# Kernel tuning notes

Hardware: AMD Instinct MI355X
Metric: run time of the kernel (lower is better)

Reference implementation:

```python
import jax, jax.numpy as jnp
import numpy as np

C = 64
CQ = C // 4
G = 8  # group norm groups
EPS_GN = 1e-5
POS_COEF = 0.1


def setup_inputs() -> dict:
    key = jax.random.key(0)
    ks = jax.random.split(key, 12)
    B, N = 2, 4096
    return {
        "context_features": jax.random.normal(ks[0], (B, C, N), jnp.float32),
        "motion_features": jax.random.normal(ks[1], (B, C, N), jnp.float32),
        "xyz1": jax.random.uniform(ks[2], (B, N, 3), jnp.float32),
        # tied q/k conv weight (Conv1d k=1, no bias): (C//4, C)
        "Wqk": jax.random.normal(ks[3], (CQ, C), jnp.float32) * 0.1,
        # v_conv: Conv1d(C, C, 1) with bias
        "Wv": jax.random.normal(ks[4], (C, C), jnp.float32) * 0.1,
        "bv": jax.random.normal(ks[5], (C,), jnp.float32) * 0.1,
        # trans_conv: Conv1d(C, C, 1) with bias
        "Wt": jax.random.normal(ks[6], (C, C), jnp.float32) * 0.1,
        "bt": jax.random.normal(ks[7], (C,), jnp.float32) * 0.1,
        # GroupNorm(8, C) affine params
        "gn_w": jax.random.normal(ks[8], (C,), jnp.float32) * 0.1 + 1.0,
        "gn_b": jax.random.normal(ks[9], (C,), jnp.float32) * 0.1,
        # PReLU single slope, alpha_gma scalar (init 0 in torch; random here for testing)
        "prelu_a": jnp.float32(0.25) + jax.random.normal(ks[10], (), jnp.float32) * 0.01,
        "alpha": jax.random.normal(ks[11], (), jnp.float32) * 0.1,
    }


def _group_norm(x, w, b):
    # x: (B, C, N)
    B, Cc, N = x.shape
    xg = x.reshape(B, G, Cc // G, N)
    mu = xg.mean(axis=(2, 3), keepdims=True)
    var = xg.var(axis=(2, 3), keepdims=True)
    xn = ((xg - mu) * jax.lax.rsqrt(var + EPS_GN)).reshape(B, Cc, N)
    return xn * w[None, :, None] + b[None, :, None]


def reference(context_features, motion_features, xyz1, Wqk, Wv, bv, Wt, bt, gn_w, gn_b, prelu_a, alpha):
    # --- self attention (tied q/k) ---
    q = jnp.einsum("oc,bcn->bon", Wqk, context_features)  # (B, C/4, N)
    corr = jnp.einsum("bom,bon->bmn", q, q)               # (B, N, N)
    attn = jax.nn.softmax(corr, axis=-1)
    attn = attn / (1e-9 + attn.sum(axis=1, keepdims=True))

    # --- position mask via Gram-trick squared distances ---
    sq = jnp.sum(xyz1 * xyz1, axis=-1)                    # (B, N)
    d = sq[:, :, None] + sq[:, None, :] - 2.0 * jnp.einsum("bid,bjd->bij", xyz1, xyz1)
    d = jnp.maximum(d, 0.0)
    pos_am = d / (1e-9 + d.sum(axis=1, keepdims=True))
    mask = pos_am <= POS_COEF

    local = attn * mask
    local = jax.nn.softmax(local, axis=-1)
    local = local / (1e-9 + local.sum(axis=1, keepdims=True))
    attn = attn + local

    # --- GMA fusion ---
    xv = jnp.einsum("oc,bcn->bon", Wv, motion_features) + bv[None, :, None]
    gma = jnp.einsum("bcm,bmn->bcn", xv, attn)
    res = jnp.einsum("oc,bcn->bon", Wt, motion_features - gma) + bt[None, :, None]
    gr = _group_norm(res, gn_w, gn_b)
    gr = jnp.where(gr >= 0, gr, prelu_a * gr)  # PReLU
    return alpha * gr + motion_features
```

## Files before the change

### kernel.cpp

```cpp
#include <hip/hip_runtime.h>
#include <hip/hip_bf16.h>
#include <cstdio>

#define NB 2
#define NN 4096
#define NC 64
#define NQ 16
#define POS_COEF 0.1f

#define OFF_QT   0u
#define OFF_QK   131072u
#define OFF_XYZ4 262144u
#define OFF_XYZK 294912u
#define OFF_IRS1 327680u
#define OFF_IRS2 335872u
#define OFF_THR  344064u
#define OFF_ICS1 352256u
#define OFF_FLAG 360448u
#define OFF_XVB  360464u
#define OFF_SUMS 622608u
#define OFF_GN   622616u
#define OFF_CS2  622648u
#define OFF_GMA  630840u
#define OFF_G2   1155128u
// ... 242 lines not shown
    const float* __restrict__ irs1, const float* __restrict__ ics1,
    const float* __restrict__ thr, float* __restrict__ irs2) {
  const int tid = threadIdx.x;
  const int b = blockIdx.x >> 8;
  const int m0 = (blockIdx.x & 255) << 4;
  const int w = tid >> 6, lane = tid & 63;
  const float* qb = qt + (size_t)b * NN * 16;
  const float* kb = qk + (size_t)b * 16 * NN;
  const float* xk = xyzk + (size_t)b * 4 * NN;
  const int mA = m0 + w, mB = m0 + w + 4, mC = m0 + w + 8, mD = m0 + w + 12;
  LQROW(ma, qb + (size_t)mA * 16)
  LQROW(mb, qb + (size_t)mB * 16)
  LQROW(mc, qb + (size_t)mC * 16)
  LQROW(md, qb + (size_t)mD * 16)
  const float4 pmA = *(const float4*)(xyz4 + ((size_t)b * NN + mA) * 4);
  const float4 pmB = *(const float4*)(xyz4 + ((size_t)b * NN + mB) * 4);
  const float4 pmC = *(const float4*)(xyz4 + ((size_t)b * NN + mC) * 4);
  const float4 pmD = *(const float4*)(xyz4 + ((size_t)b * NN + mD) * 4);
  const float rA = irs1[b * NN + mA];
  const float rB = irs1[b * NN + mB];
  const float rC = irs1[b * NN + mC];
  const float rD = irs1[b * NN + mD];
  float sA = 0.f, sB = 0.f, sC = 0.f, sD = 0.f;
#define P3C(S, M0,M1,M2,M3, PM, R, C) { \
    float corr_ = DOTC(M0,M1,M2,M3,C); \
    float a1v_ = __expf(fminf(corr_, 80.f)) * (R) * ic.C; \
    float dd_ = (PM).w + pw.C - 2.f * ((PM).x * px.C + (PM).y * py.C + (PM).z * pz.C); \
    dd_ = fmaxf(dd_, 0.f); \
    float l0_ = (dd_ <= th.C) ? a1v_ : 0.f; \
    S += __expf(l0_); }
  for (int it = 0; it < 16; ++it) {
    const int n0 = (it << 8) + (lane << 2);
    LKPL(kb, n0)
    const float4 px = *(const float4*)(xk + 0*NN + n0);
    const float4 py = *(const float4*)(xk + 1*NN + n0);
    const float4 pz = *(const float4*)(xk + 2*NN + n0);
    const float4 pw = *(const float4*)(xk + 3*NN + n0);
    const float4 ic = *(const float4*)(ics1 + b * NN + n0);
    const float4 th = *(const float4*)(thr + b * NN + n0);
    P3C(sA, ma0,ma1,ma2,ma3, pmA, rA, x)
    P3C(sA, ma0,ma1,ma2,ma3, pmA, rA, y)
    P3C(sA, ma0,ma1,ma2,ma3, pmA, rA, z)
    P3C(sA, ma0,ma1,ma2,ma3, pmA, rA, w)
    P3C(sB, mb0,mb1,mb2,mb3, pmB, rB, x)
    P3C(sB, mb0,mb1,mb2,mb3, pmB, rB, y)
    P3C(sB, mb0,mb1,mb2,mb3, pmB, rB, z)
    P3C(sB, mb0,mb1,mb2,mb3, pmB, rB, w)
    P3C(sC, mc0,mc1,mc2,mc3, pmC, rC, x)
    P3C(sC, mc0,mc1,mc2,mc3, pmC, rC, y)
    P3C(sC, mc0,mc1,mc2,mc3, pmC, rC, z)
    P3C(sC, mc0,mc1,mc2,mc3, pmC, rC, w)
    P3C(sD, md0,md1,md2,md3, pmD, rD, x)
    P3C(sD, md0,md1,md2,md3, pmD, rD, y)
    P3C(sD, md0,md1,md2,md3, pmD, rD, z)
    P3C(sD, md0,md1,md2,md3, pmD, rD, w)
  }
#undef P3C
  WRED(sA) WRED(sB) WRED(sC) WRED(sD)
  if (lane == 0) {
    irs2[b * NN + mA] = rcpf_(sA);
    irs2[b * NN + mB] = rcpf_(sB);
    irs2[b * NN + mC] = rcpf_(sC);
    irs2[b * NN + mD] = rcpf_(sD);
  }
}

__global__ __launch_bounds__(256) void k7_gma(
    const float* __restrict__ qt, const float* __restrict__ xyz4,
    const unsigned short* __restrict__ xvb,
    const float* __restrict__ irs1, const float* __restrict__ irs2,
    const float* __restrict__ ics1, const float* __restrict__ thr,
    float* __restrict__ g1, float* __restrict__ g2, float* __restrict__ cs2) {
  const int tid = threadIdx.x;
  const int bid = blockIdx.x;
  const int msl = bid & 7;
  const int nb = (bid >> 3) & 63;
  const int b = bid >> 9;
  const int n0 = nb << 6;
  const int mstart = msl << 9;
  __shared__ __align__(16) unsigned short attns1[64 * 72];
  __shared__ __align__(16) unsigned short attns2[64 * 72];
  __shared__ __align__(16) unsigned short xvs[64 * 72];
  const float* qb = qt + (size_t)b * NN * 16;
  const float* pb = xyz4 + (size_t)b * NN * 4;
  const int ni = tid & 63, aw = tid >> 6;
  const int na = n0 + ni;
  const float* qnp = qb + (size_t)na * 16;
  LQROW(q, qnp)
  const float4 pn = *(const float4*)(pb + (size_t)na * 4);
  const float ics1n = ics1[b * NN + na];
  const float thr_n = thr[b * NN + na];
  const int lane = tid & 63, wv = tid >> 6;
  const int lr = lane & 15, quad = lane >> 4;
  const int nw = wv << 4;
  f32x4v acc0 = {0,0,0,0}, acc1 = {0,0,0,0}, acc2 = {0,0,0,0}, acc3 = {0,0,0,0};
  f32x4v d0 = {0,0,0,0}, d1 = {0,0,0,0}, d2 = {0,0,0,0}, d3 = {0,0,0,0};
  float csacc = 0.f;
#define COMPA(MOFF, D1, D2) { \
    const int m_ = __builtin_amdgcn_readfirstlane(mw + (MOFF)); \
    const float* qm_ = qb + (size_t)m_ * 16; \
    LQROW(wq, qm_) \
    float corr_ = DOT16M(q0, q1, q2, q3, wq0, wq1, wq2, wq3); \
    const float4 pm_ = *(const float4*)(pb + (size_t)m_ * 4); \
    float a1v_ = __expf(fminf(corr_, 80.f)) * irs1[b * NN + m_] * ics1n; \
    float dd_ = pm_.w + pn.w - 2.f * (pm_.x * pn.x + pm_.y * pn.y + pm_.z * pn.z); \
    dd_ = fmaxf(dd_, 0.f); \
    float l0_ = (dd_ <= thr_n) ? a1v_ : 0.f; \
    float l2n_ = __expf(l0_) * irs2[b * NN + m_]; \
    D1 = f2bf(a1v_); D2 = f2bf(l2n_); csacc += l2n_; }
  for (int mt = 0; mt < 8; ++mt) {
    const int m0 = mstart + (mt << 6);
    __syncthreads();
    {
      const int c = tid >> 2, part = tid & 3;
      const unsigned short* src = xvb + ((size_t)b * 64 + c) * NN + m0 + part * 16;
      unsigned short* dst = xvs + c * 72 + part * 16;
      *(uint4*)dst = *(const uint4*)src;
      *(uint4*)(dst + 8) = *(const uint4*)(src + 8);
    }
    const int mw = m0 + (aw << 4);
#pragma unroll
    for (int g = 0; g < 4; ++g) {
      ushort4 u1, u2;
      COMPA(g * 4 + 0, u1.x, u2.x)
      COMPA(g * 4 + 1, u1.y, u2.y)
      COMPA(g * 4 + 2, u1.z, u2.z)
      COMPA(g * 4 + 3, u1.w, u2.w)
      *(ushort4*)(attns1 + ni * 72 + (aw << 4) + (g << 2)) = u1;
      *(ushort4*)(attns2 + ni * 72 + (aw << 4) + (g << 2)) = u2;
    }
    __syncthreads();
#pragma unroll
    for (int h = 0; h < 2; ++h) {
      const bf16x8 a1 = *(const bf16x8*)(attns1 + (nw + lr) * 72 + h * 32 + quad * 8);
      const bf16x8 a2 = *(const bf16x8*)(attns2 + (nw + lr) * 72 + h * 32 + quad * 8);
      const bf16x8 b0 = *(const bf16x8*)(xvs + (lr) * 72 + h * 32 + quad * 8);
      const bf16x8 b1 = *(const bf16x8*)(xvs + (16 + lr) * 72 + h * 32 + quad * 8);
      const bf16x8 b2 = *(const bf16x8*)(xvs + (32 + lr) * 72 + h * 32 + quad * 8);
      const bf16x8 b3 = *(const bf16x8*)(xvs + (48 + lr) * 72 + h * 32 + quad * 8);
      acc0 = __builtin_amdgcn_mfma_f32_16x16x32_bf16(a1, b0, acc0, 0, 0, 0);
      acc1 = __builtin_amdgcn_mfma_f32_16x16x32_bf16(a1, b1, acc1, 0, 0, 0);
      acc2 = __builtin_amdgcn_mfma_f32_16x16x32_bf16(a1, b2, acc2, 0, 0, 0);
      acc3 = __builtin_amdgcn_mfma_f32_16x16x32_bf16(a1, b3, acc3, 0, 0, 0);
      d0 = __builtin_amdgcn_mfma_f32_16x16x32_bf16(a2, b0, d0, 0, 0, 0);
      d1 = __builtin_amdgcn_mfma_f32_16x16x32_bf16(a2, b1, d1, 0, 0, 0);
      d2 = __builtin_amdgcn_mfma_f32_16x16x32_bf16(a2, b2, d2, 0, 0, 0);
      d3 = __builtin_amdgcn_mfma_f32_16x16x32_bf16(a2, b3, d3, 0, 0, 0);
    }
  }
#undef COMPA
  atomicAdd(&cs2[b * NN + na], csacc);
#define EPI(ACC, DST, CT) { \
    float* g_ = (DST) + ((size_t)b * NN + n0 + nw + (quad << 2)) * 64 + (CT) * 16 + lr; \
    atomicAdd(g_ + 0,   ACC[0]); \
    atomicAdd(g_ + 64,  ACC[1]); \
    atomicAdd(g_ + 128, ACC[2]); \
    atomicAdd(g_ + 192, ACC[3]); }
  EPI(acc0, g1, 0) EPI(acc1, g1, 1) EPI(acc2, g1, 2) EPI(acc3, g1, 3)
  EPI(d0, g2, 0) EPI(d1, g2, 1) EPI(d2, g2, 2) EPI(d3, g2, 3)
#undef EPI
}


__global__ __launch_bounds__(256) void p1w_rs1(
    const float* __restrict__ qt, const float* __restrict__ qk,
    float* __restrict__ irs1, unsigned short* __restrict__ a0g) {
  const int tid = threadIdx.x;
  const int b = blockIdx.x >> 8;
  const int m0 = (blockIdx.x & 255) << 4;
  const int w = tid >> 6, lane = tid & 63;
  const float* qb = qt + (size_t)b * NN * 16;
  const float* kb = qk + (size_t)b * 16 * NN;
  unsigned short* ab = a0g + (size_t)b * NN * NN;
  const int mA = m0 + w, mB = m0 + w + 4, mC = m0 + w + 8, mD = m0 + w + 12;
  LQROW(ma, qb + (size_t)mA * 16)
  LQROW(mb, qb + (size_t)mB * 16)
  LQROW(mc, qb + (size_t)mC * 16)
  LQROW(md, qb + (size_t)mD * 16)
  float sA = 0.f, sB = 0.f, sC = 0.f, sD = 0.f;
#define P1E(S, U, UC, M0,M1,M2,M3, C) { \
    float e_ = __expf(fminf(DOTC(M0,M1,M2,M3,C), 80.f)); \
    unsigned short us_ = f2bf(e_); U.UC = us_; S += bf2f(us_); }
  for (int it = 0; it < 16; ++it) {
    const int n0 = (it << 8) + (lane << 2);
    LKPL(kb, n0)
    ushort4 uA, uB, uC, uD;
    P1E(sA, uA, x, ma0,ma1,ma2,ma3, x) P1E(sA, uA, y, ma0,ma1,ma2,ma3, y)
    P1E(sA, uA, z, ma0,ma1,ma2,ma3, z) P1E(sA, uA, w, ma0,ma1,ma2,ma3, w)
    P1E(sB, uB, x, mb0,mb1,mb2,mb3, x) P1E(sB, uB, y, mb0,mb1,mb2,mb3, y)
    P1E(sB, uB, z, mb0,mb1,mb2,mb3, z) P1E(sB, uB, w, mb0,mb1,mb2,mb3, w)
    P1E(sC, uC, x, mc0,mc1,mc2,mc3, x) P1E(sC, uC, y, mc0,mc1,mc2,mc3, y)
    P1E(sC, uC, z, mc0,mc1,mc2,mc3, z) P1E(sC, uC, w, mc0,mc1,mc2,mc3, w)
    P1E(sD, uD, x, md0,md1,md2,md3, x) P1E(sD, uD, y, md0,md1,md2,md3, y)
    P1E(sD, uD, z, md0,md1,md2,md3, z) P1E(sD, uD, w, md0,md1,md2,md3, w)
    *(ushort4*)(ab + (size_t)mA * NN + n0) = uA;
    *(ushort4*)(ab + (size_t)mB * NN + n0) = uB;
    *(ushort4*)(ab + (size_t)mC * NN + n0) = uC;
    *(ushort4*)(ab + (size_t)mD * NN + n0) = uD;
  }
#undef P1E
  WRED(sA) WRED(sB) WRED(sC) WRED(sD)
  if (lane == 0) {
    irs1[b * NN + mA] = rcpf_(sA);
    irs1[b * NN + mB] = rcpf_(sB);
    irs1[b * NN + mC] = rcpf_(sC);
    irs1[b * NN + mD] = rcpf_(sD);
  }
}

__global__ __launch_bounds__(256) void p2r_cs1(
    const unsigned short* __restrict__ a0g, const float* __restrict__ irs1,
    float* __restrict__ ics1) {
  const int tid = threadIdx.x;
  const int w = tid >> 6, l = tid & 63;
  const int bi = blockIdx.x;
  const int b = bi >> 10;
  const int n = ((bi & 1023) << 2) + w;
  const unsigned short* row = a0g + ((size_t)b * NN + n) * NN;
  const float* ir = irs1 + b * NN;
  float s = 0.f;
#pragma unroll
  for (int it = 0; it < 8; ++it) {
    const int m = (it << 9) + (l << 3);
    const uint4 u = *(const uint4*)(row + m);
    const float4 i0 = *(const float4*)(ir + m);
    const float4 i1 = *(const float4*)(ir + m + 4);
    s = fmaf(bf2f((unsigned short)(u.x & 0xffffu)), i0.x, s);
    s = fmaf(bf2f((unsigned short)(u.x >> 16)),     i0.y, s);
    s = fmaf(bf2f((unsigned short)(u.y & 0xffffu)), i0.z, s);
    s = fmaf(bf2f((unsigned short)(u.y >> 16)),     i0.w, s);
    s = fmaf(bf2f((unsigned short)(u.z & 0xffffu)), i1.x, s);
    s = fmaf(bf2f((unsigned short)(u.z >> 16)),     i1.y, s);
    s = fmaf(bf2f((unsigned short)(u.w & 0xffffu)), i1.z, s);
    s = fmaf(bf2f((unsigned short)(u.w >> 16)),     i1.w, s);
  }
  WRED(s)
  if (l == 0) ics1[b * NN + n] = rcpf_(1e-9f + s);
}

__global__ __launch_bounds__(256) void p3w_rs2(
    const float* __restrict__ xyz4, const float* __restrict__ xyzk,
    const float* __restrict__ irs1, const float* __restrict__ ics1,
    const float* __restrict__ thr, float* __restrict__ irs2,
    const unsigned short* __restrict__ a0g, unsigned short* __restrict__ aeg) {
  const int tid = threadIdx.x;
  const int b = blockIdx.x >> 8;
  const int m0 = (blockIdx.x & 255) << 4;
  const int w = tid >> 6, lane = tid & 63;
  const float* xk = xyzk + (size_t)b * 4 * NN;
  const unsigned short* ab = a0g + (size_t)b * NN * NN;
  unsigned short* eb = aeg + (size_t)b * NN * NN;
  const int mA = m0 + w, mB = m0 + w + 4, mC = m0 + w + 8, mD = m0 + w + 12;
  const float4 pmA = *(const float4*)(xyz4 + ((size_t)b * NN + mA) * 4);
  const float4 pmB = *(const float4*)(xyz4 + ((size_t)b * NN + mB) * 4);
  const float4 pmC = *(const float4*)(xyz4 + ((size_t)b * NN + mC) * 4);
  const float4 pmD = *(const float4*)(xyz4 + ((size_t)b * NN + mD) * 4);
  const float rA = irs1[b * NN + mA];
  const float rB = irs1[b * NN + mB];
  const float rC = irs1[b * NN + mC];
  const float rD = irs1[b * NN + mD];
  float sA = 0.f, sB = 0.f, sC = 0.f, sD = 0.f;
#define P3W(S, RU, EU, UC, PM, R, C) { \
    float a1v_ = bf2f(RU.UC) * (R) * ic.C; \
    float dd_ = (PM).w + pw.C - 2.f * ((PM).x * px.C + (PM).y * py.C + (PM).z * pz.C); \
    dd_ = fmaxf(dd_, 0.f); \
    float l0_ = (dd_ <= th.C) ? a1v_ : 0.f; \
    unsigned short us_ = f2bf(__expf(l0_)); EU.UC = us_; S += bf2f(us_); }
  for (int it = 0; it < 16; ++it) {
    const int n0 = (it << 8) + (lane << 2);
    const float4 px = *(const float4*)(xk + 0*NN + n0);
    const float4 py = *(const float4*)(xk + 1*NN + n0);
    const float4 pz = *(const float4*)(xk + 2*NN + n0);
    const float4 pw = *(const float4*)(xk + 3*NN + n0);
    const float4 ic = *(const float4*)(ics1 + b * NN + n0);
    const float4 th = *(const float4*)(thr + b * NN + n0);
    const ushort4 rA4 = *(const ushort4*)(ab + (size_t)mA * NN + n0);
    const ushort4 rB4 = *(const ushort4*)(ab + (size_t)mB * NN + n0);
    const ushort4 rC4 = *(const ushort4*)(ab + (size_t)mC * NN + n0);
    const ushort4 rD4 = *(const ushort4*)(ab + (size_t)mD * NN + n0);
    ushort4 eA, eB, eC, eD;
    P3W(sA, rA4, eA, x, pmA, rA, x) P3W(sA, rA4, eA, y, pmA, rA, y)
    P3W(sA, rA4, eA, z, pmA, rA, z) P3W(sA, rA4, eA, w, pmA, rA, w)
    P3W(sB, rB4, eB, x, pmB, rB, x) P3W(sB, rB4, eB, y, pmB, rB, y)
    P3W(sB, rB4, eB, z, pmB, rB, z) P3W(sB, rB4, eB, w, pmB, rB, w)
    P3W(sC, rC4, eC, x, pmC, rC, x) P3W(sC, rC4, eC, y, pmC, rC, y)
    P3W(sC, rC4, eC, z, pmC, rC, z) P3W(sC, rC4, eC, w, pmC, rC, w)
    P3W(sD, rD4, eD, x, pmD, rD, x) P3W(sD, rD4, eD, y, pmD, rD, y)
    P3W(sD, rD4, eD, z, pmD, rD, z) P3W(sD, rD4, eD, w, pmD, rD, w)
    *(ushort4*)(eb + (size_t)mA * NN + n0) = eA;
    *(ushort4*)(eb + (size_t)mB * NN + n0) = eB;
    *(ushort4*)(eb + (size_t)mC * NN + n0) = eC;
    *(ushort4*)(eb + (size_t)mD * NN + n0) = eD;
  }
#undef P3W
  WRED(sA) WRED(sB) WRED(sC) WRED(sD)
  if (lane == 0) {
    irs2[b * NN + mA] = rcpf_(sA);
    irs2[b * NN + mB] = rcpf_(sB);
    irs2[b * NN + mC] = rcpf_(sC);
    irs2[b * NN + mD] = rcpf_(sD);
  }
}

__global__ __launch_bounds__(256) void k7n_gma(
    const unsigned short* __restrict__ a0g, const unsigned short* __restrict__ aeg,
    const unsigned short* __restrict__ xvb,
    const float* __restrict__ irs1, const float* __restrict__ irs2,
    float* __restrict__ g1, float* __restrict__ g2, float* __restrict__ cs2) {
  const int tid = threadIdx.x;
  const int bid = blockIdx.x;
  const int msl = bid & 7;
  const int nb = (bid >> 3) & 63;
  const int b = bid >> 9;
  const int n0 = nb << 6;
  const int mstart = msl << 9;
  __shared__ __align__(16) unsigned short attns1[64 * 64];
  __shared__ __align__(16) unsigned short attns2[64 * 64];
  __shared__ __align__(16) unsigned short xvs[64 * 64];
  const unsigned short* ab = a0g + (size_t)b * NN * NN;
  const unsigned short* ebp = aeg + (size_t)b * NN * NN;
  const float* irs1b = irs1 + b * NN;
  const float* irs2b = irs2 + b * NN;
  const int w = tid >> 6, l = tid & 63;
  const int lrow0 = (w << 4) + ((l >> 3) << 1);
  const int nc8 = (l & 7) << 3;
  const int gcol = n0 + nc8;
  const int xc = tid >> 2, xpart = tid & 3;
  const unsigned short* xvp = xvb + ((size_t)b * 64 + xc) * NN;
  const int lr = l & 15, quad = l >> 4;
  const int nw = w << 4;
  f32x4v acc0 = {0,0,0,0}, acc1 = {0,0,0,0}, acc2 = {0,0,0,0}, acc3 = {0,0,0,0};
  f32x4v d0 = {0,0,0,0}, d1 = {0,0,0,0}, d2 = {0,0,0,0}, d3 = {0,0,0,0};
  float csp = 0.f;

  uint4 pa0, pa1, pe0, pe1, pv0, pv1;
  float r1a, r1b, r2a, r2b;

#define ISSUE(MT) { \
    const int m0_ = mstart + ((MT) << 6); \
    const size_t ra_ = (size_t)(m0_ + lrow0) * NN + gcol; \
    pa0 = *(const uint4*)(ab + ra_); \
    pa1 = *(const uint4*)(ab + ra_ + NN); \
    pe0 = *(const uint4*)(ebp + ra_); \
    pe1 = *(const uint4*)(ebp + ra_ + NN); \
    pv0 = *(const uint4*)(xvp + m0_ + (xpart << 4)); \
    pv1 = *(const uint4*)(xvp + m0_ + (xpart << 4) + 8); \
    r1a = irs1b[m0_ + lrow0]; r1b = irs1b[m0_ + lrow0 + 1]; \
    r2a = irs2b[m0_ + lrow0]; r2b = irs2b[m0_ + lrow0 + 1]; }

#define CVW(D0, D1, SH, J, R0, R1, ARR) { \
    const float v0_ = bf2f((unsigned short)(((D0) >> (SH)) & 0xffffu)) * (R0); \
    const float v1_ = bf2f((unsigned short)(((D1) >> (SH)) & 0xffffu)) * (R1); \
    const unsigned pk_ = (unsigned)f2bf(v0_) | ((unsigned)f2bf(v1_) << 16); \
    *(unsigned*)((char*)(ARR) + ((((nc8 + (J)) << 7) + (lrow0 << 1)) ^ ((J) << 4))) = pk_; }

#define WR8(U0, U1, R0, R1, ARR) \
    CVW(U0.x, U1.x, 0,  0, R0, R1, ARR) CVW(U0.x, U1.x, 16, 1, R0, R1, ARR) \
    CVW(U0.y, U1.y, 0,  2, R0, R1, ARR) CVW(U0.y, U1.y, 16, 3, R0, R1, ARR) \
    CVW(U0.z, U1.z, 0,  4, R0, R1, ARR) CVW(U0.z, U1.z, 16, 5, R0, R1, ARR) \
    CVW(U0.w, U1.w, 0,  6, R0, R1, ARR) CVW(U0.w, U1.w, 16, 7, R0, R1, ARR)

#define LDSW(ARR, ROW, H, Q) \
    (*(const bf16x8*)((const char*)(ARR) + \
      ((((ROW) << 7) + ((H) << 6) + ((Q) << 4)) ^ (((ROW) & 7) << 4))))

  ISSUE(0)
  for (int mt = 0; mt < 8; ++mt) {
    __syncthreads();
    WR8(pa0, pa1, r1a, r1b, attns1)
    WR8(pe0, pe1, r2a, r2b, attns2)
    {
      const int xb = (xc << 7) + (xpart << 5);
      const int xs = (xc & 7) << 4;
      *(uint4*)((char*)xvs + ((xb) ^ xs)) = pv0;
      *(uint4*)((char*)xvs + ((xb + 16) ^ xs)) = pv1;
    }
    __syncthreads();
    if (mt < 7) ISSUE(mt + 1)
#pragma unroll
    for (int h = 0; h < 2; ++h) {
      const bf16x8 a1 = LDSW(attns1, nw + lr, h, quad);
      const bf16x8 a2 = LDSW(attns2, nw + lr, h, quad);
      const bf16x8 b0 = LDSW(xvs, lr, h, quad);
      const bf16x8 b1 = LDSW(xvs, 16 + lr, h, quad);
      const bf16x8 b2 = LDSW(xvs, 32 + lr, h, quad);
      const bf16x8 b3 = LDSW(xvs, 48 + lr, h, quad);
      acc0 = __builtin_amdgcn_mfma_f32_16x16x32_bf16(a1, b0, acc0, 0, 0, 0);
      acc1 = __builtin_amdgcn_mfma_f32_16x16x32_bf16(a1, b1, acc1, 0, 0, 0);
      acc2 = __builtin_amdgcn_mfma_f32_16x16x32_bf16(a1, b2, acc2, 0, 0, 0);
      acc3 = __builtin_amdgcn_mfma_f32_16x16x32_bf16(a1, b3, acc3, 0, 0, 0);
      d0 = __builtin_amdgcn_mfma_f32_16x16x32_bf16(a2, b0, d0, 0, 0, 0);
      d1 = __builtin_amdgcn_mfma_f32_16x16x32_bf16(a2, b1, d1, 0, 0, 0);
      d2 = __builtin_amdgcn_mfma_f32_16x16x32_bf16(a2, b2, d2, 0, 0, 0);
      d3 = __builtin_amdgcn_mfma_f32_16x16x32_bf16(a2, b3, d3, 0, 0, 0);
#pragma unroll
      for (int j = 0; j < 8; ++j) csp += bf2f((unsigned short)a2[j]);
    }
  }
#undef ISSUE
#undef CVW
#undef WR8
#undef LDSW
  csp += __shfl_xor(csp, 32);
  csp += __shfl_xor(csp, 16);
  if (quad == 0) atomicAdd(&cs2[b * NN + n0 + nw + lr], csp);
#define EPI(ACC, DST, CT) { \
    float* g_ = (DST) + ((size_t)b * NN + n0 + nw + (quad << 2)) * 64 + (CT) * 16 + lr; \
    atomicAdd(g_ + 0,   ACC[0]); \
    atomicAdd(g_ + 64,  ACC[1]); \
    atomicAdd(g_ + 128, ACC[2]); \
    atomicAdd(g_ + 192, ACC[3]); }
  EPI(acc0, g1, 0) EPI(acc1, g1, 1) EPI(acc2, g1, 2) EPI(acc3, g1, 3)
  EPI(d0, g2, 0) EPI(d1, g2, 1) EPI(d2, g2, 2) EPI(d3, g2, 3)
#undef EPI
}


__global__ __launch_bounds__(256) void p2_cs1(
    const float* __restrict__ qt, const float* __restrict__ qk,
    const float* __restrict__ irs1, float* __restrict__ ics1) {
  const int tid = threadIdx.x;
  const int b = blockIdx.x >> 8;
  const int n0t = (blockIdx.x & 255) << 4;
  const int w = tid >> 6, lane = tid & 63;
  const float* qb = qt + (size_t)b * NN * 16;
  const float* kb = qk + (size_t)b * 16 * NN;
  const int nA = n0t + w, nB = n0t + w + 4, nC = n0t + w + 8, nD = n0t + w + 12;
  LQROW(na, qb + (size_t)nA * 16)
  LQROW(nb, qb + (size_t)nB * 16)
  LQROW(nc, qb + (size_t)nC * 16)
  LQROW(nd, qb + (size_t)nD * 16)
  float sA = 0.f, sB = 0.f, sC = 0.f, sD = 0.f;
  for (int it = 0; it < 16; ++it) {
    const int m0 = (it << 8) + (lane << 2);
    LKPL(kb, m0)
    const float4 r1 = *(const float4*)(irs1 + b * NN + m0);
    sA = fmaf(__expf(fminf(DOTC(na0,na1,na2,na3,x), 80.f)), r1.x, sA);
    sA = fmaf(__expf(fminf(DOTC(na0,na1,na2,na3,y), 80.f)), r1.y, sA);
    sA = fmaf(__expf(fminf(DOTC(na0,na1,na2,na3,z), 80.f)), r1.z, sA);
    sA = fmaf(__expf(fminf(DOTC(na0,na1,na2,na3,w), 80.f)), r1.w, sA);
    sB = fmaf(__expf(fminf(DOTC(nb0,nb1,nb2,nb3,x), 80.f)), r1.x, sB);
    sB = fmaf(__expf(fminf(DOTC(nb0,nb1,nb2,nb3,y), 80.f)), r1.y, sB);
    sB = fmaf(__expf(fminf(DOTC(nb0,nb1,nb2,nb3,z), 80.f)), r1.z, sB);
    sB = fmaf(__expf(fminf(DOTC(nb0,nb1,nb2,nb3,w), 80.f)), r1.w, sB);
    sC = fmaf(__expf(fminf(DOTC(nc0,nc1,nc2,nc3,x), 80.f)), r1.x, sC);
    sC = fmaf(__expf(fminf(DOTC(nc0,nc1,nc2,nc3,y), 80.f)), r1.y, sC);
    sC = fmaf(__expf(fminf(DOTC(nc0,nc1,nc2,nc3,z), 80.f)), r1.z, sC);
    sC = fmaf(__expf(fminf(DOTC(nc0,nc1,nc2,nc3,w), 80.f)), r1.w, sC);
    sD = fmaf(__expf(fminf(DOTC(nd0,nd1,nd2,nd3,x), 80.f)), r1.x, sD);
    sD = fmaf(__expf(fminf(DOTC(nd0,nd1,nd2,nd3,y), 80.f)), r1.y, sD);
    sD = fmaf(__expf(fminf(DOTC(nd0,nd1,nd2,nd3,z), 80.f)), r1.z, sD);
    sD = fmaf(__expf(fminf(DOTC(nd0,nd1,nd2,nd3,w), 80.f)), r1.w, sD);
  }
  WRED(sA) WRED(sB) WRED(sC) WRED(sD)
  if (lane == 0) {
    ics1[b * NN + nA] = rcpf_(1e-9f + sA);
    ics1[b * NN + nB] = rcpf_(1e-9f + sB);
    ics1[b * NN + nC] = rcpf_(1e-9f + sC);
    ics1[b * NN + nD] = rcpf_(1e-9f + sD);
  }
}

__global__ __launch_bounds__(256) void k8_res(
    const void* __restrict__ mot, const void* __restrict__ wt,
    const void* __restrict__ bt, const float* __restrict__ flag,
    float* __restrict__ g1_res, const float* __restrict__ g2,
    const float* __restrict__ cs2, float* __restrict__ gn,
    const float* __restrict__ ics1, int g1mode) {
  const bool f32 = flag[0] > 0.5f;
  const int tid = threadIdx.x;
  const int bid = blockIdx.x;
  const int b = bid >> 9;
  const int n0 = (bid & 511) << 3;
  __shared__ float wtT[64 * 65];
  __shared__ float bts[64];
  __shared__ float md[8 * 64];
  __shared__ float gs[8], gss[8];
  for (int i = tid; i < 4096; i += 256) {
    int o = i & 63, c = i >> 6;
    wtT[c * 65 + o] = ldin(wt, o * 64 + c, f32);
  }
  if (tid < 64) bts[tid] = ldin(bt, tid, f32);
  if (tid < 8) { gs[tid] = 0.f; gss[tid] = 0.f; }
#pragma unroll
  for (int r = 0; r < 2; ++r) {
    const int idx = tid * 2 + r;
    const int c = idx & 63, nl = idx >> 6;
    const size_t gi = ((size_t)b * NN + n0 + nl) * 64 + c;
    const float ics2n = rcpf_(1e-9f + cs2[b * NN + n0 + nl]);
    float g1v = g1_res[gi];
    if (g1mode) g1v *= ics1[b * NN + n0 + nl];
    float gmav = fmaf(g2[gi], ics2n, g1v);
    md[nl * 64 + c] = ldin(mot, ((size_t)b * 64 + c) * NN + n0 + nl, f32) - gmav;
  }
  __syncthreads();
  const int o = tid & 63, ng = tid >> 6;
  const int nl0 = ng * 2, nl1 = ng * 2 + 1;
  float a0 = bts[o], a1 = bts[o];
#pragma unroll 8
  for (int c = 0; c < 64; ++c) {
    float w = wtT[c * 65 + o];
    a0 = fmaf(w, md[nl0 * 64 + c], a0);
    a1 = fmaf(w, md[nl1 * 64 + c], a1);
  }
  g1_res[((size_t)b * NN + n0 + nl0) * 64 + o] = a0;
  g1_res[((size_t)b * NN + n0 + nl1) * 64 + o] = a1;
  atomicAdd(&gs[o >> 3], a0 + a1);
  atomicAdd(&gss[o >> 3], a0 * a0 + a1 * a1);
  __syncthreads();
  if (tid < 8) atomicAdd(&gn[b * 8 + tid], gs[tid]);
  else if (tid < 16) atomicAdd(&gn[16 + b * 8 + (tid - 8)], gss[tid - 8]);
}

__global__ __launch_bounds__(256) void k9_out(
    const float* __restrict__ res, const float* __restrict__ gn,
    const void* __restrict__ mot,
    const void* __restrict__ gnw, const void* __restrict__ gnb,
    const void* __restrict__ pa, const void* __restrict__ al,
    const float* __restrict__ flag, void* __restrict__ out) {
  const bool f32 = flag[0] > 0.5f;
  const int idx = blockIdx.x * 256 + threadIdx.x;
  const int n = idx & 4095;
  const int c = (idx >> 12) & 63;
  const int b = idx >> 18;
  const int g = c >> 3;
  const float inv_cnt = 1.f / 32768.f;
  float mean = gn[b * 8 + g] * inv_cnt;
  float var = gn[16 + b * 8 + g] * inv_cnt - mean * mean;
  var = fmaxf(var, 0.f);
  float rstd = rsqrtf(var + 1e-5f);
  float r = res[((size_t)b * NN + n) * 64 + c];
  float y = (r - mean) * rstd * ldin(gnw, c, f32) + ldin(gnb, c, f32);
  float slope = ldin(pa, 0, f32);
  y = (y >= 0.f) ? y : slope * y;
  float o = ldin(al, 0, f32) * y + ldin(mot, idx, f32);
  if (f32) ((float*)out)[idx] = o;
  else     ((__hip_bfloat16*)out)[idx] = __float2bfloat16(o);
}

extern "C" void kernel_launch(void* const* d_in, const int* in_sizes, int n_in,
                              void* d_out, int out_size, void* d_ws, size_t ws_size,
                              hipStream_t stream) {
  const void* ctx = d_in[0];
  const void* mot = d_in[1];
  const void* xyz = d_in[2];
  const void* wqk = d_in[3];
  const void* wv  = d_in[4];
  const void* bv  = d_in[5];
  const void* wt  = d_in[6];
  const void* bt  = d_in[7];
  const void* gnw = d_in[8];
  const void* gnb = d_in[9];
  const void* pa  = d_in[10];
  const void* al  = d_in[11];
  float* ws = (float*)d_ws;
  const bool big = ws_size >= (size_t)FULL_F * sizeof(float);

  if (ws_size < (size_t)WS_TOTAL * sizeof(float))
    fprintf(stderr, "[gma3d] WARNING ws_size=%zu < needed %zu\n",
            ws_size, (size_t)WS_TOTAL * sizeof(float));

  hipMemsetAsync(ws + OFF_SUMS, 0, (size_t)ZERO_F * sizeof(float), stream);

  k0_detect<<<1, 256, 0, stream>>>((const unsigned short*)ctx, ws + OFF_FLAG);
  k1_q_xyz<<<32, 256, 0, stream>>>(ctx, xyz, wqk, ws + OFF_FLAG,
                                   ws + OFF_QT, ws + OFF_QK,
                                   ws + OFF_XYZ4, ws + OFF_XYZK, ws + OFF_SUMS);
  k2_xv<<<128, 256, 0, stream>>>(mot, wv, bv, ws + OFF_FLAG,
                                 (unsigned short*)(ws + OFF_XVB));
  k2b_thr<<<32, 256, 0, stream>>>(ws + OFF_XYZ4, ws + OFF_SUMS, ws + OFF_THR);

  if (big) {
    unsigned short* a0 = (unsigned short*)(ws + OFF_A0);
    unsigned short* ae = (unsigned short*)(ws + OFF_AE);
    p1w_rs1<<<512, 256, 0, stream>>>(ws + OFF_QT, ws + OFF_QK, ws + OFF_IRS1, a0);
    p2r_cs1<<<2048, 256, 0, stream>>>(a0, ws + OFF_IRS1, ws + OFF_ICS1);
    p3w_rs2<<<512, 256, 0, stream>>>(ws + OFF_XYZ4, ws + OFF_XYZK,
                                     ws + OFF_IRS1, ws + OFF_ICS1, ws + OFF_THR,
                                     ws + OFF_IRS2, a0, ae);
    k7n_gma<<<1024, 256, 0, stream>>>(a0, ae,
                                      (const unsigned short*)(ws + OFF_XVB),
                                      ws + OFF_IRS1, ws + OFF_IRS2,
                                      ws + OFF_GMA, ws + OFF_G2, ws + OFF_CS2);
    k8_res<<<1024, 256, 0, stream>>>(mot, wt, bt, ws + OFF_FLAG,
                                     ws + OFF_GMA, ws + OFF_G2, ws + OFF_CS2,
                                     ws + OFF_GN, ws + OFF_ICS1, 1);
  } else {
    p1_rs1<<<512, 256, 0, stream>>>(ws + OFF_QT, ws + OFF_QK, ws + OFF_IRS1);
    p2_cs1<<<512, 256, 0, stream>>>(ws + OFF_QT, ws + OFF_QK, ws + OFF_IRS1, ws + OFF_ICS1);
    p3_rs2<<<512, 256, 0, stream>>>(ws + OFF_QT, ws + OFF_QK,
                                    ws + OFF_XYZ4, ws + OFF_XYZK,
                                    ws + OFF_IRS1, ws + OFF_ICS1, ws + OFF_THR,
                                    ws + OFF_IRS2);
    k7_gma<<<1024, 256, 0, stream>>>(ws + OFF_QT, ws + OFF_XYZ4,
                                     (const unsigned short*)(ws + OFF_XVB),
                                     ws + OFF_IRS1, ws + OFF_IRS2,
                                     ws + OFF_ICS1, ws + OFF_THR,
                                     ws + OFF_GMA, ws + OFF_G2, ws + OFF_CS2);
    k8_res<<<1024, 256, 0, stream>>>(mot, wt, bt, ws + OFF_FLAG,
                                     ws + OFF_GMA, ws + OFF_G2, ws + OFF_CS2,
                                     ws + OFF_GN, ws + OFF_ICS1, 0);
  }

  k9_out<<<2048, 256, 0, stream>>>(ws + OFF_GMA, ws + OFF_GN, mot, gnw, gnb, pa, al,
                                   ws + OFF_FLAG, d_out);
}
```

Measured before the change: 306.0 us.

## Double-buffer GMA tiles, precompute column sums, fold normalization into single epilogue

Result: faster. 299.0 us (-2.3%).

```diff
diff --git a/kernel.cpp b/kernel.cpp
--- a/kernel.cpp
+++ b/kernel.cpp
@@ -568,21 +568,48 @@
   }
 }
 
+__global__ __launch_bounds__(256) void p4_cs2(
+    const unsigned short* __restrict__ aeg, const float* __restrict__ irs2,
+    float* __restrict__ cs2) {
+  const int tid = threadIdx.x;
+  const int bid = blockIdx.x;
+  const int ms = bid & 15;
+  const int ng = (bid >> 4) & 7;
+  const int b  = bid >> 7;
+  const int n2 = (ng << 9) + (tid << 1);
+  const unsigned short* eb = aeg + (size_t)b * NN * NN + n2;
+  const float* r2 = irs2 + b * NN;
+  float s0 = 0.f, s1 = 0.f;
+  const int m0 = ms << 8;
+#pragma unroll 4
+  for (int m = m0; m < m0 + 256; ++m) {
+    const unsigned u = *(const unsigned*)(eb + (size_t)m * NN);
+    const float r = r2[m];
+    s0 += bf2f(f2bf(bf2f((unsigned short)(u & 0xffffu)) * r));
+    s1 += bf2f(f2bf(bf2f((unsigned short)(u >> 16)) * r));
+  }
+  atomicAdd(&cs2[b * NN + n2], s0);
+  atomicAdd(&cs2[b * NN + n2 + 1], s1);
+}
+
+#define SW(r) ((((r) & 7) << 4) ^ ((((r) >> 3) & 3) << 5))
+
 __global__ __launch_bounds__(256) void k7n_gma(
     const unsigned short* __restrict__ a0g, const unsigned short* __restrict__ aeg,
     const unsigned short* __restrict__ xvb,
     const float* __restrict__ irs1, const float* __restrict__ irs2,
-    float* __restrict__ g1, float* __restrict__ g2, float* __restrict__ cs2) {
+    const float* __restrict__ ics1, const float* __restrict__ cs2,
+    float* __restrict__ gma) {
   const int tid = threadIdx.x;
   const int bid = blockIdx.x;
-  const int msl = bid & 7;
-  const int nb = (bid >> 3) & 63;
-  const int b = bid >> 9;
+  const int msl = bid & 3;
+  const int nb  = (bid >> 2) & 63;
+  const int b   = bid >> 8;
   const int n0 = nb << 6;
-  const int mstart = msl << 9;
-  __shared__ __align__(16) unsigned short attns1[64 * 64];
-  __shared__ __align__(16) unsigned short attns2[64 * 64];
-  __shared__ __align__(16) unsigned short xvs[64 * 64];
+  const int mstart = msl << 10;
+  __shared__ __align__(16) unsigned short attns1[2][64 * 64];
+  __shared__ __align__(16) unsigned short attns2[2][64 * 64];
+  __shared__ __align__(16) unsigned short xvs[2][64 * 64];
   const unsigned short* ab = a0g + (size_t)b * NN * NN;
   const unsigned short* ebp = aeg + (size_t)b * NN * NN;
   const float* irs1b = irs1 + b * NN;
@@ -597,28 +624,29 @@
   const int nw = w << 4;
   f32x4v acc0 = {0,0,0,0}, acc1 = {0,0,0,0}, acc2 = {0,0,0,0}, acc3 = {0,0,0,0};
   f32x4v d0 = {0,0,0,0}, d1 = {0,0,0,0}, d2 = {0,0,0,0}, d3 = {0,0,0,0};
-  float csp = 0.f;
-
-  uint4 pa0, pa1, pe0, pe1, pv0, pv1;
-  float r1a, r1b, r2a, r2b;
-
-#define ISSUE(MT) { \
+
+  uint4 pa0A, pa1A, pe0A, pe1A, pv0A, pv1A;
+  uint4 pa0B, pa1B, pe0B, pe1B, pv0B, pv1B;
+  float r1aA, r1bA, r2aA, r2bA, r1aB, r1bB, r2aB, r2bB;
+
+#define ISSUE(S, MT) { \
     const int m0_ = mstart + ((MT) << 6); \
     const size_t ra_ = (size_t)(m0_ + lrow0) * NN + gcol; \
-    pa0 = *(const uint4*)(ab + ra_); \
-    pa1 = *(const uint4*)(ab + ra_ + NN); \
-    pe0 = *(const uint4*)(ebp + ra_); \
-    pe1 = *(const uint4*)(ebp + ra_ + NN); \
-    pv0 = *(const uint4*)(xvp + m0_ + (xpart << 4)); \
-    pv1 = *(const uint4*)(xvp + m0_ + (xpart << 4) + 8); \
-    r1a = irs1b[m0_ + lrow0]; r1b = irs1b[m0_ + lrow0 + 1]; \
-    r2a = irs2b[m0_ + lrow0]; r2b = irs2b[m0_ + lrow0 + 1]; }
+    pa0##S = *(const uint4*)(ab + ra_); \
+    pa1##S = *(const uint4*)(ab + ra_ + NN); \
+    pe0##S = *(const uint4*)(ebp + ra_); \
+    pe1##S = *(const uint4*)(ebp + ra_ + NN); \
+    pv0##S = *(const uint4*)(xvp + m0_ + (xpart << 4)); \
+    pv1##S = *(const uint4*)(xvp + m0_ + (xpart << 4) + 8); \
+    r1a##S = irs1b[m0_ + lrow0]; r1b##S = irs1b[m0_ + lrow0 + 1]; \
+    r2a##S = irs2b[m0_ + lrow0]; r2b##S = irs2b[m0_ + lrow0 + 1]; }
 
 #define CVW(D0, D1, SH, J, R0, R1, ARR) { \
     const float v0_ = bf2f((unsigned short)(((D0) >> (SH)) & 0xffffu)) * (R0); \
     const float v1_ = bf2f((unsigned short)(((D1) >> (SH)) & 0xffffu)) * (R1); \
     const unsigned pk_ = (unsigned)f2bf(v0_) | ((unsigned)f2bf(v1_) << 16); \
-    *(unsigned*)((char*)(ARR) + ((((nc8 + (J)) << 7) + (lrow0 << 1)) ^ ((J) << 4))) = pk_; }
+    const int nl_ = nc8 + (J); \
+    *(unsigned*)((char*)(ARR) + ((((nl_) << 7) + (lrow0 << 1)) ^ SW(nl_))) = pk_; }
 
 #define WR8(U0, U1, R0, R1, ARR) \
     CVW(U0.x, U1.x, 0,  0, R0, R1, ARR) CVW(U0.x, U1.x, 16, 1, R0, R1, ARR) \
@@ -626,58 +654,70 @@
     CVW(U0.z, U1.z, 0,  4, R0, R1, ARR) CVW(U0.z, U1.z, 16, 5, R0, R1, ARR) \
     CVW(U0.w, U1.w, 0,  6, R0, R1, ARR) CVW(U0.w, U1.w, 16, 7, R0, R1, ARR)
 
+#define STX(XARR, PV0, PV1) { \
+    const int xb_ = (xc << 7) + (xpart << 5); \
+    *(uint4*)((char*)(XARR) + ((xb_) ^ SW(xc))) = PV0; \
+    *(uint4*)((char*)(XARR) + ((xb_ + 16) ^ SW(xc))) = PV1; }
+
 #define LDSW(ARR, ROW, H, Q) \
     (*(const bf16x8*)((const char*)(ARR) + \
-      ((((ROW) << 7) + ((H) << 6) + ((Q) << 4)) ^ (((ROW) & 7) << 4))))
-
-  ISSUE(0)
-  for (int mt = 0; mt < 8; ++mt) {
+      ((((ROW) << 7) + ((H) << 6) + ((Q) << 4)) ^ SW(ROW))))
+
+#define MPH(A1P, A2P, XVP_) { \
+    for (int h = 0; h < 2; ++h) { \
+      const bf16x8 fa1 = LDSW(A1P, nw + lr, h, quad); \
+      const bf16x8 fa2 = LDSW(A2P, nw + lr, h, quad); \
+      const bf16x8 fb0 = LDSW(XVP_, lr, h, quad); \
+      const bf16x8 fb1 = LDSW(XVP_, 16 + lr, h, quad); \
+      const bf16x8 fb2 = LDSW(XVP_, 32 + lr, h, quad); \
+      const bf16x8 fb3 = LDSW(XVP_, 48 + lr, h, quad); \
+      acc0 = __builtin_amdgcn_mfma_f32_16x16x32_bf16(fa1, fb0, acc0, 0, 0, 0); \
+      acc1 = __builtin_amdgcn_mfma_f32_16x16x32_bf16(fa1, fb1, acc1, 0, 0, 0); \
+      acc2 = __builtin_amdgcn_mfma_f32_16x16x32_bf16(fa1, fb2, acc2, 0, 0, 0); \
+      acc3 = __builtin_amdgcn_mfma_f32_16x16x32_bf16(fa1, fb3, acc3, 0, 0, 0); \
+      d0 = __builtin_amdgcn_mfma_f32_16x16x32_bf16(fa2, fb0, d0, 0, 0, 0); \
+      d1 = __builtin_amdgcn_mfma_f32_16x16x32_bf16(fa2, fb1, d1, 0, 0, 0); \
+      d2 = __builtin_amdgcn_mfma_f32_16x16x32_bf16(fa2, fb2, d2, 0, 0, 0); \
+      d3 = __builtin_amdgcn_mfma_f32_16x16x32_bf16(fa2, fb3, d3, 0, 0, 0); \
+    } }
+
+  ISSUE(A, 0)
+  ISSUE(B, 1)
+  for (int mt = 0; mt < 16; mt += 2) {
+    WR8(pa0A, pa1A, r1aA, r1bA, attns1[0])
+    WR8(pe0A, pe1A, r2aA, r2bA, attns2[0])
+    STX(xvs[0], pv0A, pv1A)
     __syncthreads();
-    WR8(pa0, pa1, r1a, r1b, attns1)
-    WR8(pe0, pe1, r2a, r2b, attns2)
-    {
-      const int xb = (xc << 7) + (xpart << 5);
-      const int xs = (xc & 7) << 4;
-      *(uint4*)((char*)xvs + ((xb) ^ xs)) = pv0;
-      *(uint4*)((char*)xvs + ((xb + 16) ^ xs)) = pv1;
-    }
+    if (mt + 2 < 16) { ISSUE(A, mt + 2) }
+    MPH(attns1[0], attns2[0], xvs[0])
+    WR8(pa0B, pa1B, r1aB, r1bB, attns1[1])
+    WR8(pe0B, pe1B, r2aB, r2bB, attns2[1])
+    STX(xvs[1], pv0B, pv1B)
     __syncthreads();
-    if (mt < 7) ISSUE(mt + 1)
-#pragma unroll
-    for (int h = 0; h < 2; ++h) {
-      const bf16x8 a1 = LDSW(attns1, nw + lr, h, quad);
-      const bf16x8 a2 = LDSW(attns2, nw + lr, h, quad);
-      const bf16x8 b0 = LDSW(xvs, lr, h, quad);
-      const bf16x8 b1 = LDSW(xvs, 16 + lr, h, quad);
-      const bf16x8 b2 = LDSW(xvs, 32 + lr, h, quad);
-      const bf16x8 b3 = LDSW(xvs, 48 + lr, h, quad);
-      acc0 = __builtin_amdgcn_mfma_f32_16x16x32_bf16(a1, b0, acc0, 0, 0, 0);
-      acc1 = __builtin_amdgcn_mfma_f32_16x16x32_bf16(a1, b1, acc1, 0, 0, 0);
-      acc2 = __builtin_amdgcn_mfma_f32_16x16x32_bf16(a1, b2, acc2, 0, 0, 0);
-      acc3 = __builtin_amdgcn_mfma_f32_16x16x32_bf16(a1, b3, acc3, 0, 0, 0);
-      d0 = __builtin_amdgcn_mfma_f32_16x16x32_bf16(a2, b0, d0, 0, 0, 0);
-      d1 = __builtin_amdgcn_mfma_f32_16x16x32_bf16(a2, b1, d1, 0, 0, 0);
-      d2 = __builtin_amdgcn_mfma_f32_16x16x32_bf16(a2, b2, d2, 0, 0, 0);
-      d3 = __builtin_amdgcn_mfma_f32_16x16x32_bf16(a2, b3, d3, 0, 0, 0);
-#pragma unroll
-      for (int j = 0; j < 8; ++j) csp += bf2f((unsigned short)a2[j]);
-    }
+    if (mt + 3 < 16) { ISSUE(B, mt + 3) }
+    MPH(attns1[1], attns2[1], xvs[1])
   }
 #undef ISSUE
 #undef CVW
 #undef WR8
+#undef STX
 #undef LDSW
-  csp += __shfl_xor(csp, 32);
-  csp += __shfl_xor(csp, 16);
-  if (quad == 0) atomicAdd(&cs2[b * NN + n0 + nw + lr], csp);
-#define EPI(ACC, DST, CT) { \
-    float* g_ = (DST) + ((size_t)b * NN + n0 + nw + (quad << 2)) * 64 + (CT) * 16 + lr; \
-    atomicAdd(g_ + 0,   ACC[0]); \
-    atomicAdd(g_ + 64,  ACC[1]); \
-    atomicAdd(g_ + 128, ACC[2]); \
-    atomicAdd(g_ + 192, ACC[3]); }
-  EPI(acc0, g1, 0) EPI(acc1, g1, 1) EPI(acc2, g1, 2) EPI(acc3, g1, 3)
-  EPI(d0, g2, 0) EPI(d1, g2, 1) EPI(d2, g2, 2) EPI(d3, g2, 3)
+#undef MPH
+  float w10, w11, w12, w13, w20, w21, w22, w23;
+  {
+    const int nr = n0 + nw + (quad << 2);
+    w10 = ics1[b * NN + nr + 0]; w20 = rcpf_(1e-9f + cs2[b * NN + nr + 0]);
+    w11 = ics1[b * NN + nr + 1]; w21 = rcpf_(1e-9f + cs2[b * NN + nr + 1]);
+    w12 = ics1[b * NN + nr + 2]; w22 = rcpf_(1e-9f + cs2[b * NN + nr + 2]);
+    w13 = ics1[b * NN + nr + 3]; w23 = rcpf_(1e-9f + cs2[b * NN + nr + 3]);
+  }
+#define EPI(ACC, DD, CT) { \
+    float* g_ = gma + ((size_t)b * NN + n0 + nw + (quad << 2)) * 64 + (CT) * 16 + lr; \
+    atomicAdd(g_ + 0,   fmaf(ACC[0], w10, DD[0] * w20)); \
+    atomicAdd(g_ + 64,  fmaf(ACC[1], w11, DD[1] * w21)); \
+    atomicAdd(g_ + 128, fmaf(ACC[2], w12, DD[2] * w22)); \
+    atomicAdd(g_ + 192, fmaf(ACC[3], w13, DD[3] * w23)); }
+  EPI(acc0, d0, 0) EPI(acc1, d1, 1) EPI(acc2, d2, 2) EPI(acc3, d3, 3)
 #undef EPI
 }
 
@@ -753,10 +793,15 @@
     const int idx = tid * 2 + r;
     const int c = idx & 63, nl = idx >> 6;
     const size_t gi = ((size_t)b * NN + n0 + nl) * 64 + c;
-    const float ics2n = rcpf_(1e-9f + cs2[b * NN + n0 + nl]);
-    float g1v = g1_res[gi];
-    if (g1mode) g1v *= ics1[b * NN + n0 + nl];
-    float gmav = fmaf(g2[gi], ics2n, g1v);
+    float gmav;
+    if (g1mode == 2) {
+      gmav = g1_res[gi];
+    } else {
+      const float ics2n = rcpf_(1e-9f + cs2[b * NN + n0 + nl]);
+      float g1v = g1_res[gi];
+      if (g1mode == 1) g1v *= ics1[b * NN + n0 + nl];
+      gmav = fmaf(g2[gi], ics2n, g1v);
+    }
     md[nl * 64 + c] = ldin(mot, ((size_t)b * 64 + c) * NN + n0 + nl, f32) - gmav;
   }
   __syncthreads();
@@ -844,13 +889,15 @@
     p3w_rs2<<<512, 256, 0, stream>>>(ws + OFF_XYZ4, ws + OFF_XYZK,
                                      ws + OFF_IRS1, ws + OFF_ICS1, ws + OFF_THR,
                                      ws + OFF_IRS2, a0, ae);
-    k7n_gma<<<1024, 256, 0, stream>>>(a0, ae,
-                                      (const unsigned short*)(ws + OFF_XVB),
-                                      ws + OFF_IRS1, ws + OFF_IRS2,
-                                      ws + OFF_GMA, ws + OFF_G2, ws + OFF_CS2);
+    p4_cs2<<<256, 256, 0, stream>>>(ae, ws + OFF_IRS2, ws + OFF_CS2);
+    k7n_gma<<<512, 256, 0, stream>>>(a0, ae,
+                                     (const unsigned short*)(ws + OFF_XVB),
+                                     ws + OFF_IRS1, ws + OFF_IRS2,
+                                     ws + OFF_ICS1, ws + OFF_CS2,
+                                     ws + OFF_GMA);
     k8_res<<<1024, 256, 0, stream>>>(mot, wt, bt, ws + OFF_FLAG,
                                      ws + OFF_GMA, ws + OFF_G2, ws + OFF_CS2,
-                                     ws + OFF_GN, ws + OFF_ICS1, 1);
+                                     ws + OFF_GN, ws + OFF_ICS1, 2);
   } else {
     p1_rs1<<<512, 256, 0, stream>>>(ws + OFF_QT, ws + OFF_QK, ws + OFF_IRS1);
     p2_cs1<<<512, 256, 0, stream>>>(ws + OFF_QT, ws + OFF_QK, ws + OFF_IRS1, ws + OFF_ICS1);
```
